# Kernel tuning notes

Hardware: AMD Instinct MI355X
Metric: run time of the kernel (lower is better)

The kernel has to match this reference:

```python
import jax, jax.numpy as jnp
import numpy as np

TEMPERATURE = 0.5


def setup_inputs() -> dict:
    key = jax.random.key(0)
    k1, k2 = jax.random.split(key)
    N, D = 4096, 128
    z_i = jax.random.normal(k1, (N, D), dtype=jnp.float32)
    z_j = jax.random.normal(k2, (N, D), dtype=jnp.float32)
    return {"z_i": z_i, "z_j": z_j}


def reference(z_i, z_j):
    # make_permutation interleaves the two views: rows are
    # [z_i[0], z_j[0], z_i[1], z_j[1], ...]  -> shape [2N, D]
    N, D = z_i.shape
    z = jnp.stack([z_i, z_j], axis=1).reshape(2 * N, D)
    # cosine similarity: zTz / (||z_a|| * ||z_b||) == normalized rows matmul
    norm = jnp.linalg.norm(z, axis=-1, keepdims=True)  # [2N, 1]
    s = (z @ z.T) / (norm @ norm.T)                    # [2N, 2N]
    e = jnp.exp(s / TEMPERATURE)
    idx = jnp.arange(2 * N)
    partner = idx ^ 1                                   # (2k <-> 2k+1) positive pairs
    numerator = e[idx, partner]                         # [2N]
    denominator = jnp.sum(e, axis=-1) - jnp.diagonal(e)  # row-sum minus self-sim
    # original sums all 2N per-sample losses then divides by 2N == mean
    return jnp.mean(-jnp.log(numerator / denominator))
```

## Files before the change

### kernel.cpp

```cpp
#include <hip/hip_runtime.h>
#include <hip/hip_bf16.h>

#define N_PAIR 4096
#define N_ROW  8192
#define DIM    128
#define NX     8

typedef __attribute__((ext_vector_type(4))) float f32x4;
typedef __attribute__((ext_vector_type(4))) int   i32x4;
typedef __attribute__((ext_vector_type(8))) int   i32x8;

__device__ inline float fast_exp2(float x) {
#if __has_builtin(__builtin_amdgcn_exp2f)
    return __builtin_amdgcn_exp2f(x);
#else
    float r; asm("v_exp_f32 %0, %1" : "=v"(r) : "v"(x)); return r;
#endif
}
__device__ inline float fast_log2(float x) {
#if __has_builtin(__builtin_amdgcn_logf)
    return __builtin_amdgcn_logf(x);
#else
    float r; asm("v_log_f32 %0, %1" : "=v"(r) : "v"(x)); return r;
#endif
}

__global__ __launch_bounds__(256) void k_prep(const float* __restrict__ zi,
                                              const float* __restrict__ zj,
                                              unsigned char* __restrict__ zh8,
                                              float* __restrict__ pd,
                                              float* __restrict__ rowsum) {
    const int wid  = threadIdx.x >> 6;
    const int lane = threadIdx.x & 63;
    const int k    = blockIdx.x * 4 + wid;
    float2 a = *(const float2*)&zi[k * DIM + lane * 2];
    float2 b = *(const float2*)&zj[k * DIM + lane * 2];
    float ssi = a.x * a.x + a.y * a.y;
    float ssj = b.x * b.x + b.y * b.y;
    float dot = a.x * b.x + a.y * b.y;
#pragma unroll
    for (int off = 1; off < 64; off <<= 1) {
        ssi += __shfl_xor(ssi, off);
        ssj += __shfl_xor(ssj, off);
        dot += __shfl_xor(dot, off);
    }
    const float invi = rsqrtf(ssi), invj = rsqrtf(ssj);
    unsigned int pi = __builtin_amdgcn_cvt_pk_fp8_f32(a.x * invi, a.y * invi, 0, false);
    unsigned int pj = __builtin_amdgcn_cvt_pk_fp8_f32(b.x * invj, b.y * invj, 0, false);
    ((unsigned short*)zh8)[(2 * k)     * (DIM / 2) + lane] = (unsigned short)pi;
    ((unsigned short*)zh8)[(2 * k + 1) * (DIM / 2) + lane] = (unsigned short)pj;
    if (lane == 0) {
        pd[k] = dot * invi * invj;
        rowsum[2 * k]     = 0.f;
        rowsum[2 * k + 1] = 0.f;
    }
}

__global__ __launch_bounds__(512, 4) void k_simsum(const unsigned char* __restrict__ zh8,
                                                   float* __restrict__ rowsum) {
    __shared__ unsigned char Bs[8 * 8192];
    __shared__ float rsum_lds[128];
    const int tid  = threadIdx.x;
    const int lane = tid & 63;
    const int wid  = tid >> 6;
    const int wr   = wid >> 2, wc = wid & 3;
    const int l15  = lane & 15, lhi = lane >> 4;
    const int by   = blockIdx.y;
    const int bx0  = blockIdx.x * NX;
    const int row0 = by * 128 + wr * 64;
    const int wbase = wid * 8192;

    if (tid < 128) rsum_lds[tid] = 0.f;
    __syncthreads();

    i32x8 a[4];
#pragma unroll
    for (int m = 0; m < 4; ++m) {
        const unsigned char* ap = &zh8[(row0 + m * 16 + l15) * DIM + lhi * 32];
        union { i32x4 h[2]; i32x8 v; } u;
        u.h[0] = *(const i32x4*)ap;
        u.h[1] = *(const i32x4*)(ap + 16);
        a[m] = u.v;
    }

    auto stage = [&](int ct, int buf) {
#pragma unroll
        for (int i = 0; i < 4; ++i) {
            const int rl = i * 8 + (lane >> 3);
            const int g  = (lane & 7) ^ (rl & 7);
            const unsigned char* src = zh8 + (ct * 128 + wc * 32 + rl) * DIM + g * 16;
            __builtin_amdgcn_global_load_lds(
                (const __attribute__((address_space(1))) void*)src,
                (__attribute__((address_space(3))) void*)(&Bs[wbase + buf * 4096 + i * 1024]),
                16, 0, 0);
        }
    };

    const float K2E = 2.8853900817779268f;
    const int   SC1 = 0x7F7F7F7F;
    float rs[4] = {0.f, 0.f, 0.f, 0.f};

    stage(bx0, 0);
    asm volatile("s_waitcnt vmcnt(0)" ::: "memory");

    int cur = 0;
#pragma unroll 1
    for (int t = 0; t < NX; ++t) {
        if (t + 1 < NX) stage(bx0 + t + 1, cur ^ 1);
        const int bx = bx0 + t;
        i32x8 b[2];
#pragma unroll
        for (int n = 0; n < 2; ++n) {
            const int rowb = n * 16 + l15;
            const int base = wbase + cur * 4096 + rowb * 128;
            union { i32x4 h[2]; i32x8 v; } u;
            u.h[0] = *(const i32x4*)&Bs[base + (((lhi * 2 + 0) ^ (l15 & 7)) << 4)];
            u.h[1] = *(const i32x4*)&Bs[base + (((lhi * 2 + 1) ^ (l15 & 7)) << 4)];
            b[n] = u.v;
        }
        f32x4 accT[2][4];
        __builtin_amdgcn_s_setprio(1);
#pragma unroll
        for (int n = 0; n < 2; ++n)
#pragma unroll
            for (int m = 0; m < 4; ++m)
                accT[n][m] = __builtin_amdgcn_mfma_scale_f32_16x16x128_f8f6f4(
                    b[n], a[m], (f32x4){0.f, 0.f, 0.f, 0.f},
                    0, 0,
                    0, SC1, 0, SC1);
        __builtin_amdgcn_s_setprio(0);
        if (bx == by) {
#pragma unroll
            for (int m = 0; m < 4; ++m) {
                const int rloc = wr * 64 + m * 16 + l15;
                float s0 = 0.f, s1 = 0.f;
#pragma unroll
                for (int n = 0; n < 2; ++n)
#pragma unroll
                    for (int r = 0; r < 4; ++r) {
                        const int cloc = wc * 32 + n * 16 + lhi * 4 + r;
                        float v = fast_exp2(K2E * accT[n][m][r]);
                        v = (cloc == rloc) ? 0.f : v;
                        if (n == 0) s0 += v; else s1 += v;
                    }
                rs[m] += s0 + s1;
            }
        } else {
#pragma unroll
            for (int m = 0; m < 4; ++m) {
                float s0 = 0.f, s1 = 0.f;
#pragma unroll
                for (int n = 0; n < 2; ++n)
#pragma unroll
                    for (int r = 0; r < 4; ++r) {
                        float v = fast_exp2(K2E * accT[n][m][r]);
                        if (n == 0) s0 += v; else s1 += v;
                    }
                rs[m] += s0 + s1;
            }
        }
        if (t + 1 < NX) {
            asm volatile("s_waitcnt vmcnt(0)" ::: "memory");
            cur ^= 1;
        }
    }

#pragma unroll
    for (int m = 0; m < 4; ++m) {
        rs[m] += __shfl_xor(rs[m], 16);
        rs[m] += __shfl_xor(rs[m], 32);
    }
    if (lane < 16) {
#pragma unroll
        for (int m = 0; m < 4; ++m)
            atomicAdd(&rsum_lds[wr * 64 + m * 16 + lane], rs[m]);
    }
    __syncthreads();
    if (tid < 128) atomicAdd(&rowsum[by * 128 + tid], rsum_lds[tid]);
}

__global__ __launch_bounds__(1024) void k_loss(const float* __restrict__ rowsum,
                                               const float* __restrict__ pd,
                                               float* __restrict__ out) {
    const int tid  = threadIdx.x;
    const int lane = tid & 63;
    const int wid  = tid >> 6;
    const float LN2 = 0.6931471805599453f;
    float local = 0.f;
    for (int i = tid; i < N_ROW; i += 1024)
        local += fast_log2(rowsum[i]) * LN2 - 2.f * pd[i >> 1];
#pragma unroll
    for (int off = 1; off < 64; off <<= 1) local += __shfl_xor(local, off);
    __shared__ float wsum[16];
    if (lane == 0) wsum[wid] = local;
    __syncthreads();
    if (tid == 0) {
        float s = 0.f;
#pragma unroll
        for (int w = 0; w < 16; ++w) s += wsum[w];
        out[0] = s * (1.f / (float)N_ROW);
    }
}

extern "C" void kernel_launch(void* const* d_in, const int* in_sizes, int n_in,
                              void* d_out, int out_size, void* d_ws, size_t ws_size,
                              hipStream_t stream) {
    const float* zi = (const float*)d_in[0];
    const float* zj = (const float*)d_in[1];
    char* ws = (char*)d_ws;
    unsigned char* zh8 = (unsigned char*)ws;
    float* rowsum = (float*)(ws + 2 * 1024 * 1024);
    float* pd     = (float*)(ws + 2 * 1024 * 1024 + 32 * 1024);

    k_prep<<<N_PAIR / 4, 256, 0, stream>>>(zi, zj, zh8, pd, rowsum);
    dim3 grid(64 / NX, 64);
    k_simsum<<<grid, 512, 0, stream>>>(zh8, rowsum);
    k_loss<<<1, 1024, 0, stream>>>(rowsum, pd, (float*)d_out);
}
```

Baseline: 31.68 us.

## Load B tiles directly into registers with double-buffering instead of LDS staging

Removes the 64KB LDS staging buffer and global_load_lds path. Each wave now loads its B fragments straight from global memory into registers, ping-ponging between two register sets so the next tile's loads overlap the current tile's MFMA and exp work. This drops the LDS traffic and shared-memory footprint, which can raise occupancy, at the cost of more registers and uncoalesced per-lane global loads that depend on L2 hits.

```diff
diff --git a/kernel.cpp b/kernel.cpp
--- a/kernel.cpp
+++ b/kernel.cpp
@@ -58,7 +58,6 @@
 
 __global__ __launch_bounds__(512, 4) void k_simsum(const unsigned char* __restrict__ zh8,
                                                    float* __restrict__ rowsum) {
-    __shared__ unsigned char Bs[8 * 8192];
     __shared__ float rsum_lds[128];
     const int tid  = threadIdx.x;
     const int lane = tid & 63;
@@ -68,7 +67,6 @@
     const int by   = blockIdx.y;
     const int bx0  = blockIdx.x * NX;
     const int row0 = by * 128 + wr * 64;
-    const int wbase = wid * 8192;
 
     if (tid < 128) rsum_lds[tid] = 0.f;
     __syncthreads();
@@ -83,41 +81,23 @@
         a[m] = u.v;
     }
 
-    auto stage = [&](int ct, int buf) {
-#pragma unroll
-        for (int i = 0; i < 4; ++i) {
-            const int rl = i * 8 + (lane >> 3);
-            const int g  = (lane & 7) ^ (rl & 7);
-            const unsigned char* src = zh8 + (ct * 128 + wc * 32 + rl) * DIM + g * 16;
-            __builtin_amdgcn_global_load_lds(
-                (const __attribute__((address_space(1))) void*)src,
-                (__attribute__((address_space(3))) void*)(&Bs[wbase + buf * 4096 + i * 1024]),
-                16, 0, 0);
-        }
-    };
-
     const float K2E = 2.8853900817779268f;
     const int   SC1 = 0x7F7F7F7F;
     float rs[4] = {0.f, 0.f, 0.f, 0.f};
 
-    stage(bx0, 0);
-    asm volatile("s_waitcnt vmcnt(0)" ::: "memory");
-
-    int cur = 0;
-#pragma unroll 1
-    for (int t = 0; t < NX; ++t) {
-        if (t + 1 < NX) stage(bx0 + t + 1, cur ^ 1);
-        const int bx = bx0 + t;
-        i32x8 b[2];
+    auto loadB = [&](int ct, i32x8* b) {
 #pragma unroll
         for (int n = 0; n < 2; ++n) {
-            const int rowb = n * 16 + l15;
-            const int base = wbase + cur * 4096 + rowb * 128;
+            const unsigned char* bp =
+                zh8 + (ct * 128 + wc * 32 + n * 16 + l15) * DIM + lhi * 32;
             union { i32x4 h[2]; i32x8 v; } u;
-            u.h[0] = *(const i32x4*)&Bs[base + (((lhi * 2 + 0) ^ (l15 & 7)) << 4)];
-            u.h[1] = *(const i32x4*)&Bs[base + (((lhi * 2 + 1) ^ (l15 & 7)) << 4)];
+            u.h[0] = *(const i32x4*)bp;
+            u.h[1] = *(const i32x4*)(bp + 16);
             b[n] = u.v;
         }
+    };
+
+    auto compute = [&](int ct, const i32x8* b) {
         f32x4 accT[2][4];
         __builtin_amdgcn_s_setprio(1);
 #pragma unroll
@@ -129,7 +109,7 @@
                     0, 0,
                     0, SC1, 0, SC1);
         __builtin_amdgcn_s_setprio(0);
-        if (bx == by) {
+        if (ct == by) {
 #pragma unroll
             for (int m = 0; m < 4; ++m) {
                 const int rloc = wr * 64 + m * 16 + l15;
@@ -159,10 +139,16 @@
                 rs[m] += s0 + s1;
             }
         }
-        if (t + 1 < NX) {
-            asm volatile("s_waitcnt vmcnt(0)" ::: "memory");
-            cur ^= 1;
-        }
+    };
+
+    i32x8 bA[2], bB[2];
+    loadB(bx0, bA);
+#pragma unroll 1
+    for (int t = 0; t < NX; t += 2) {
+        if (t + 1 < NX) loadB(bx0 + t + 1, bB);
+        compute(bx0 + t, bA);
+        if (t + 2 < NX) loadB(bx0 + t + 2, bA);
+        compute(bx0 + t + 1, bB);
     }
 
 #pragma unroll
```

After: 33.37 us. 5.3% more time.
